# Optimization experiments

Measured on AMD Instinct MI355X. Metric: run time of the kernel, lower is better.

## Reference

```python
import jax, jax.numpy as jnp
import numpy as np

DMN_FACTOR = 0.5  # (2.0 - default_mode_network_activity=1.0) * 0.5, constant at default state


def setup_inputs() -> dict:
    key = jax.random.key(0)
    k1, k2, k3, k4 = jax.random.split(key, 4)
    B, H = 16384, 2048
    return {
        "x": jax.random.normal(k1, (B, H), dtype=jnp.float32),
        "W": jax.random.normal(k2, (H, H), dtype=jnp.float32) * (1.0 / np.sqrt(H)),
        "b": jnp.zeros((H,), dtype=jnp.float32),
        "plasticity_modulation": jax.random.uniform(k3, (H,), dtype=jnp.float32),
        "connectivity_mask": jax.random.uniform(k4, (H, H), dtype=jnp.float32),
    }


def reference(x, W, b, plasticity_modulation, connectivity_mask):
    H = x.shape[1]
    # trkb_signaling: Linear + Sigmoid
    bdnf_effect = jax.nn.sigmoid(x @ W.T + b)  # [B, H]
    # elementwise plasticity scaling
    xs = x * plasticity_modulation  # [B, H]
    # functional integration: mean_j(xs_i * xs_j * mask_ij) == xs * (mask @ xs^T)/H
    # (fused form of bmm outer-product * mask, mean over dim=2)
    fi = xs * (xs @ connectivity_mask.T) * (DMN_FACTOR / H)  # [B, H]
    return xs + bdnf_effect * fi
```

## Files before the change

kernel.cpp:

```cpp
#include <hip/hip_runtime.h>


#define M_DIM 16384
#define H_DIM 2048
#define BM 128
#define BN 128
#define BKB 128
#define NKT (H_DIM / BKB)
#define NTHREADS 512

typedef __attribute__((ext_vector_type(4))) int   intx4;
typedef __attribute__((ext_vector_type(8))) int   intx8;
typedef __attribute__((ext_vector_type(4))) float floatx4;

#define GPTR(p) ((const __attribute__((address_space(1))) void*)(p))
#define LPTR(p) ((__attribute__((address_space(3))) void*)(p))

__device__ __forceinline__ int pk4(float a, float b, float c, float d) {
    int v = __builtin_amdgcn_cvt_pk_fp8_f32(a, b, 0, false);
    v     = __builtin_amdgcn_cvt_pk_fp8_f32(c, d, v, true);
    return v;
}

__global__ void cvt_x8_kernel(const float* __restrict__ x,
                              unsigned char* __restrict__ x8, long n) {
    long stride = (long)gridDim.x * blockDim.x * 8;
    for (long j = ((long)blockIdx.x * blockDim.x + threadIdx.x) * 8; j < n; j += stride) {
        float4 v0 = *reinterpret_cast<const float4*>(x + j);
        float4 v1 = *reinterpret_cast<const float4*>(x + j + 4);
        int2 o;
        o.x = pk4(v0.x, v0.y, v0.z, v0.w);
        o.y = pk4(v1.x, v1.y, v1.z, v1.w);
        *reinterpret_cast<int2*>(x8 + j) = o;
    }
}

__global__ void cvt_wm8_kernel(const float* __restrict__ W,
                               const float* __restrict__ Mk,
                               const float* __restrict__ pm,
                               unsigned char* __restrict__ W8,
                               unsigned char* __restrict__ M8, long n) {
    long stride = (long)gridDim.x * blockDim.x * 8;
    for (long j = ((long)blockIdx.x * blockDim.x + threadIdx.x) * 8; j < n; j += stride) {
        float4 w0 = *reinterpret_cast<const float4*>(W + j);
        float4 w1 = *reinterpret_cast<const float4*>(W + j + 4);
        float4 m0 = *reinterpret_cast<const float4*>(Mk + j);
        float4 m1 = *reinterpret_cast<const float4*>(Mk + j + 4);
        const long col = j & (H_DIM - 1);
        float4 p0 = *reinterpret_cast<const float4*>(pm + col);
        float4 p1 = *reinterpret_cast<const float4*>(pm + col + 4);
        int2 ow, om;
        ow.x = pk4(w0.x * 16.f, w0.y * 16.f, w0.z * 16.f, w0.w * 16.f);
        ow.y = pk4(w1.x * 16.f, w1.y * 16.f, w1.z * 16.f, w1.w * 16.f);
        om.x = pk4(m0.x * p0.x * 16.f, m0.y * p0.y * 16.f,
                   m0.z * p0.z * 16.f, m0.w * p0.w * 16.f);
        om.y = pk4(m1.x * p1.x * 16.f, m1.y * p1.y * 16.f,
                   m1.z * p1.z * 16.f, m1.w * p1.w * 16.f);
        *reinterpret_cast<int2*>(W8 + j) = ow;
        *reinterpret_cast<int2*>(M8 + j) = om;
    }
}

__device__ __forceinline__ intx8 frag8(const unsigned char* s, int row, int g) {
    const unsigned char* p = s + row * BKB;
    const int c0 = ((2 * g)     ^ (row & 7)) * 16;
    const int c1 = ((2 * g + 1) ^ (row & 7)) * 16;
    intx4 lo = *reinterpret_cast<const intx4*>(p + c0);
    intx4 hi = *reinterpret_cast<const intx4*>(p + c1);
    return (intx8){lo.x, lo.y, lo.z, lo.w, hi.x, hi.y, hi.z, hi.w};
}

#define GLDS(src, dst) __builtin_amdgcn_global_load_lds(GPTR(src), LPTR(dst), 16, 0, 0)

#define STAGE_A(b, kt) do { \
    GLDS(gA0 + (kt),                       &sA[b][(srow     ) * BKB + scol_l]); \
    GLDS(gA0 + (kt) + (size_t)64  * H_DIM, &sA[b][(srow + 64) * BKB + scol_l]); } while (0)

#define STAGE_W(b, kt) do { \
    GLDS(gW0 + (kt),                       &sW[b][(srow     ) * BKB + scol_l]); \
    GLDS(gW0 + (kt) + (size_t)64  * H_DIM, &sW[b][(srow + 64) * BKB + scol_l]); } while (0)

#define STAGE_M(b, kt) do { \
    GLDS(gM0 + (kt),                       &sM[b][(srow     ) * BKB + scol_l]); \
    GLDS(gM0 + (kt) + (size_t)64  * H_DIM, &sM[b][(srow + 64) * BKB + scol_l]); } while (0)

#define BAR()  __builtin_amdgcn_s_barrier()
#define SBAR() __builtin_amdgcn_sched_barrier(0)
#define LGK0() do { asm volatile("s_waitcnt lgkmcnt(0)" ::: "memory"); SBAR(); } while (0)
#define VMC(n) asm volatile("s_waitcnt vmcnt(" #n ")" ::: "memory")
#define SGB(mask, n) __builtin_amdgcn_sched_group_barrier(mask, n, 0)

#define MFMASC(a, b, c) \
    __builtin_amdgcn_mfma_scale_f32_16x16x128_f8f6f4(a, b, c, 0, 0, 0, 127, 0, 123)

#define RD_A(dst, buf) do { \
    _Pragma("unroll") for (int m_ = 0; m_ < 4; ++m_) \
        dst[m_] = frag8(sA[buf], arow + m_ * 16, lg); } while (0)
#define RD_B(dst, sb, buf) do { \
    _Pragma("unroll") for (int n_ = 0; n_ < 2; ++n_) \
        dst[n_] = frag8(sb[buf], brw + n_ * 16, lg); } while (0)

#define MM(acc, av, bv) do { \
    _Pragma("unroll") for (int m_ = 0; m_ < 4; ++m_) \
    _Pragma("unroll") for (int n_ = 0; n_ < 2; ++n_) \
        acc[m_][n_] = MFMASC(av[m_], bv[n_], acc[m_][n_]); } while (0)

#define TILE(ct, nt, kst) do { \
    STAGE_A(nt, kst); STAGE_W(nt, kst); STAGE_M(nt, kst); \
    SBAR(); \
    RD_A(aF, ct); RD_B(bW, sW, ct); \
    LGK0(); \
    __builtin_amdgcn_s_setprio(1); \
    RD_B(bM, sM, ct); \
    MM(acc1, aF, bW); \
    _Pragma("unroll") for (int i_ = 0; i_ < 4; ++i_) { SGB(0x8, 1); SGB(0x100, 1); } \
    SGB(0x8, 4); \
    __builtin_amdgcn_s_setprio(0); \
    LGK0(); \
    __builtin_amdgcn_s_setprio(1); \
    MM(acc2, aF, bM); \
    __builtin_amdgcn_s_setprio(0); \
    SBAR(); \
    VMC(6); \
    BAR(); } while (0)

#define KOF(tt) (((tt) * BKB) & (H_DIM - 1))

__global__ __launch_bounds__(NTHREADS, 2)
void fused_gemm_kernel(const unsigned char* __restrict__ x8,
                       const unsigned char* __restrict__ W8,
                       const unsigned char* __restrict__ M8,
                       const float* __restrict__ x,
                       const float* __restrict__ bias,
                       const float* __restrict__ pm,
                       float* __restrict__ out) {
    __shared__ __align__(16) unsigned char sA[3][BM * BKB];
    __shared__ __align__(16) unsigned char sW[3][BN * BKB];
    __shared__ __align__(16) unsigned char sM[3][BN * BKB];

    const int t    = threadIdx.x;
    const int brow = blockIdx.y * BM;
    const int bcol = blockIdx.x * BN;

    const int srow   = t >> 3;
    const int chunk  = t & 7;
    const int scol_l = chunk * 16;
    const int scol_g = (chunk ^ (srow & 7)) * 16;

    const int w    = t >> 6;
    const int lane = t & 63;
    const int wr   = w >> 2;
    const int wc   = w & 3;
    const int lrow = lane & 15;
    const int lg   = lane >> 4;
    const int arow = wr * 64 + lrow;
    const int brw  = wc * 32 + lrow;

    floatx4 acc1[4][2], acc2[4][2];
#pragma unroll
    for (int m = 0; m < 4; ++m)
#pragma unroll
        for (int n = 0; n < 2; ++n) {
            acc1[m][n] = (floatx4){0.f, 0.f, 0.f, 0.f};
            acc2[m][n] = (floatx4){0.f, 0.f, 0.f, 0.f};
        }

    const unsigned char* gA0 = x8 + (size_t)(brow + srow) * H_DIM + scol_g;
    const unsigned char* gW0 = W8 + (size_t)(bcol + srow) * H_DIM + scol_g;
    const unsigned char* gM0 = M8 + (size_t)(bcol + srow) * H_DIM + scol_g;

    intx8 aF[4], bW[2], bM[2];

    STAGE_A(0, KOF(0)); STAGE_W(0, KOF(0)); STAGE_M(0, KOF(0));
    STAGE_A(1, KOF(1)); STAGE_W(1, KOF(1)); STAGE_M(1, KOF(1));
    VMC(6);
    BAR();

#pragma unroll 1
    for (int j = 0; j < 5; ++j) {
        const int t0 = 3 * j;
        TILE(0, 2, KOF(t0 + 2));
        TILE(1, 0, KOF(t0 + 3));
        TILE(2, 1, KOF(t0 + 4));
    }
    TILE(0, 2, KOF(17));

    const float c = 0.5f / (float)H_DIM;
#pragma unroll
    for (int n = 0; n < 2; ++n) {
        const int gcol = bcol + wc * 32 + n * 16 + lrow;
        const float bj  = bias[gcol];
        const float pmj = pm[gcol];
#pragma unroll
        for (int m = 0; m < 4; ++m) {
            floatx4 a1 = acc1[m][n];
            floatx4 a2 = acc2[m][n];
            const int growb = brow + wr * 64 + m * 16 + lg * 4;
#pragma unroll
            for (int r = 0; r < 4; ++r) {
                const size_t idx = (size_t)(growb + r) * H_DIM + gcol;
                const float xs  = x[idx] * pmj;
                const float s1  = a1[r] + bj;
                const float sig = 1.0f / (1.0f + __expf(-s1));
                out[idx] = xs + sig * (xs * a2[r] * c);
            }
        }
    }
}

extern "C" void kernel_launch(void* const* d_in, const int* in_sizes, int n_in,
                              void* d_out, int out_size, void* d_ws, size_t ws_size,
                              hipStream_t stream) {
    const float* x   = (const float*)d_in[0];
    const float* W   = (const float*)d_in[1];
    const float* b   = (const float*)d_in[2];
    const float* pm  = (const float*)d_in[3];
    const float* Mk  = (const float*)d_in[4];
    float* out = (float*)d_out;

    const long n_x = (long)M_DIM * H_DIM;
    const long n_w = (long)H_DIM * H_DIM;

    unsigned char* x8 = (unsigned char*)d_ws;
    unsigned char* W8 = x8 + n_x;
    unsigned char* M8 = W8 + n_w;

    cvt_x8_kernel<<<2048, 256, 0, stream>>>(x, x8, n_x);
    cvt_wm8_kernel<<<1024, 256, 0, stream>>>(W, Mk, pm, W8, M8, n_w);

    dim3 grid(H_DIM / BN, M_DIM / BM);
    fused_gemm_kernel<<<grid, NTHREADS, 0, stream>>>(x8, W8, M8, x, b, pm, out);
}
```

Measured before the change: 220.6 us.

## Pre-swizzle W and mask into MFMA fragment layout, load B directly to registers

```diff
diff --git a/kernel.cpp b/kernel.cpp
--- a/kernel.cpp
+++ b/kernel.cpp
@@ -8,6 +8,7 @@
 #define BKB 128
 #define NKT (H_DIM / BKB)
 #define NTHREADS 512
+#define FRAG_STRIDE 2048
 
 typedef __attribute__((ext_vector_type(4))) int   intx4;
 typedef __attribute__((ext_vector_type(8))) int   intx8;
@@ -35,30 +36,38 @@
     }
 }
 
-__global__ void cvt_wm8_kernel(const float* __restrict__ W,
-                               const float* __restrict__ Mk,
-                               const float* __restrict__ pm,
-                               unsigned char* __restrict__ W8,
-                               unsigned char* __restrict__ M8, long n) {
-    long stride = (long)gridDim.x * blockDim.x * 8;
-    for (long j = ((long)blockIdx.x * blockDim.x + threadIdx.x) * 8; j < n; j += stride) {
-        float4 w0 = *reinterpret_cast<const float4*>(W + j);
-        float4 w1 = *reinterpret_cast<const float4*>(W + j + 4);
-        float4 m0 = *reinterpret_cast<const float4*>(Mk + j);
-        float4 m1 = *reinterpret_cast<const float4*>(Mk + j + 4);
-        const long col = j & (H_DIM - 1);
-        float4 p0 = *reinterpret_cast<const float4*>(pm + col);
-        float4 p1 = *reinterpret_cast<const float4*>(pm + col + 4);
-        int2 ow, om;
-        ow.x = pk4(w0.x * 16.f, w0.y * 16.f, w0.z * 16.f, w0.w * 16.f);
-        ow.y = pk4(w1.x * 16.f, w1.y * 16.f, w1.z * 16.f, w1.w * 16.f);
-        om.x = pk4(m0.x * p0.x * 16.f, m0.y * p0.y * 16.f,
-                   m0.z * p0.z * 16.f, m0.w * p0.w * 16.f);
-        om.y = pk4(m1.x * p1.x * 16.f, m1.y * p1.y * 16.f,
-                   m1.z * p1.z * 16.f, m1.w * p1.w * 16.f);
-        *reinterpret_cast<int2*>(W8 + j) = ow;
-        *reinterpret_cast<int2*>(M8 + j) = om;
-    }
+__global__ void cvt_wm8f_kernel(const float* __restrict__ W,
+                                const float* __restrict__ Mk,
+                                const float* __restrict__ pm,
+                                unsigned char* __restrict__ W8f,
+                                unsigned char* __restrict__ M8f) {
+    const int tid = blockIdx.x * blockDim.x + threadIdx.x;
+    const int l   = tid & 63;
+    const int kt  = (tid >> 6) & (NKT - 1);
+    const int ct  = tid >> 10;
+    const int col = ct * 16 + (l & 15);
+    const int k0  = kt * 128 + (l >> 4) * 32;
+    const float* wsrc = W  + (size_t)col * H_DIM + k0;
+    const float* msrc = Mk + (size_t)col * H_DIM + k0;
+    const float* psrc = pm + k0;
+    int ow[8], om[8];
+#pragma unroll
+    for (int q = 0; q < 8; ++q) {
+        float4 wv = *reinterpret_cast<const float4*>(wsrc + q * 4);
+        float4 mv = *reinterpret_cast<const float4*>(msrc + q * 4);
+        float4 pv = *reinterpret_cast<const float4*>(psrc + q * 4);
+        ow[q] = pk4(wv.x * 16.f, wv.y * 16.f, wv.z * 16.f, wv.w * 16.f);
+        om[q] = pk4(mv.x * pv.x * 16.f, mv.y * pv.y * 16.f,
+                    mv.z * pv.z * 16.f, mv.w * pv.w * 16.f);
+    }
+    intx4 w0 = (intx4){ow[0], ow[1], ow[2], ow[3]};
+    intx4 w1 = (intx4){ow[4], ow[5], ow[6], ow[7]};
+    intx4 m0 = (intx4){om[0], om[1], om[2], om[3]};
+    intx4 m1 = (intx4){om[4], om[5], om[6], om[7]};
+    *reinterpret_cast<intx4*>(W8f + (size_t)tid * 32)      = w0;
+    *reinterpret_cast<intx4*>(W8f + (size_t)tid * 32 + 16) = w1;
+    *reinterpret_cast<intx4*>(M8f + (size_t)tid * 32)      = m0;
+    *reinterpret_cast<intx4*>(M8f + (size_t)tid * 32 + 16) = m1;
 }
 
 __device__ __forceinline__ intx8 frag8(const unsigned char* s, int row, int g) {
@@ -70,25 +79,22 @@
     return (intx8){lo.x, lo.y, lo.z, lo.w, hi.x, hi.y, hi.z, hi.w};
 }
 
+__device__ __forceinline__ intx8 ldb(const unsigned char* p) {
+    intx4 lo = *reinterpret_cast<const intx4*>(p);
+    intx4 hi = *reinterpret_cast<const intx4*>(p + 16);
+    return (intx8){lo.x, lo.y, lo.z, lo.w, hi.x, hi.y, hi.z, hi.w};
+}
+
 #define GLDS(src, dst) __builtin_amdgcn_global_load_lds(GPTR(src), LPTR(dst), 16, 0, 0)
 
 #define STAGE_A(b, kt) do { \
     GLDS(gA0 + (kt),                       &sA[b][(srow     ) * BKB + scol_l]); \
     GLDS(gA0 + (kt) + (size_t)64  * H_DIM, &sA[b][(srow + 64) * BKB + scol_l]); } while (0)
-
-#define STAGE_W(b, kt) do { \
-    GLDS(gW0 + (kt),                       &sW[b][(srow     ) * BKB + scol_l]); \
-    GLDS(gW0 + (kt) + (size_t)64  * H_DIM, &sW[b][(srow + 64) * BKB + scol_l]); } while (0)
-
-#define STAGE_M(b, kt) do { \
-    GLDS(gM0 + (kt),                       &sM[b][(srow     ) * BKB + scol_l]); \
-    GLDS(gM0 + (kt) + (size_t)64  * H_DIM, &sM[b][(srow + 64) * BKB + scol_l]); } while (0)
 
 #define BAR()  __builtin_amdgcn_s_barrier()
 #define SBAR() __builtin_amdgcn_sched_barrier(0)
 #define LGK0() do { asm volatile("s_waitcnt lgkmcnt(0)" ::: "memory"); SBAR(); } while (0)
 #define VMC(n) asm volatile("s_waitcnt vmcnt(" #n ")" ::: "memory")
-#define SGB(mask, n) __builtin_amdgcn_sched_group_barrier(mask, n, 0)
 
 #define MFMASC(a, b, c) \
     __builtin_amdgcn_mfma_scale_f32_16x16x128_f8f6f4(a, b, c, 0, 0, 0, 127, 0, 123)
@@ -96,47 +102,42 @@
 #define RD_A(dst, buf) do { \
     _Pragma("unroll") for (int m_ = 0; m_ < 4; ++m_) \
         dst[m_] = frag8(sA[buf], arow + m_ * 16, lg); } while (0)
-#define RD_B(dst, sb, buf) do { \
-    _Pragma("unroll") for (int n_ = 0; n_ < 2; ++n_) \
-        dst[n_] = frag8(sb[buf], brw + n_ * 16, lg); } while (0)
 
 #define MM(acc, av, bv) do { \
     _Pragma("unroll") for (int m_ = 0; m_ < 4; ++m_) \
     _Pragma("unroll") for (int n_ = 0; n_ < 2; ++n_) \
         acc[m_][n_] = MFMASC(av[m_], bv[n_], acc[m_][n_]); } while (0)
 
-#define TILE(ct, nt, kst) do { \
-    STAGE_A(nt, kst); STAGE_W(nt, kst); STAGE_M(nt, kst); \
-    SBAR(); \
-    RD_A(aF, ct); RD_B(bW, sW, ct); \
+#define KOF(tt) (((tt) * BKB) & (H_DIM - 1))
+
+#define TILE(ct_, nt_, tcur, tnext) do { \
+    bW[0] = ldb(bWb + (size_t)(tcur) * FRAG_STRIDE); \
+    bW[1] = ldb(bWb + (size_t)NKT * FRAG_STRIDE + (size_t)(tcur) * FRAG_STRIDE); \
+    SBAR(); \
+    bM[0] = ldb(bMb + (size_t)(tcur) * FRAG_STRIDE); \
+    bM[1] = ldb(bMb + (size_t)NKT * FRAG_STRIDE + (size_t)(tcur) * FRAG_STRIDE); \
+    SBAR(); \
+    STAGE_A(nt_, KOF(tnext)); \
+    SBAR(); \
+    RD_A(aF, ct_); \
     LGK0(); \
-    __builtin_amdgcn_s_setprio(1); \
-    RD_B(bM, sM, ct); \
-    MM(acc1, aF, bW); \
-    _Pragma("unroll") for (int i_ = 0; i_ < 4; ++i_) { SGB(0x8, 1); SGB(0x100, 1); } \
-    SGB(0x8, 4); \
-    __builtin_amdgcn_s_setprio(0); \
-    LGK0(); \
-    __builtin_amdgcn_s_setprio(1); \
-    MM(acc2, aF, bM); \
-    __builtin_amdgcn_s_setprio(0); \
-    SBAR(); \
     VMC(6); \
+    __builtin_amdgcn_s_setprio(1); MM(acc1, aF, bW); __builtin_amdgcn_s_setprio(0); \
+    VMC(2); \
+    __builtin_amdgcn_s_setprio(1); MM(acc2, aF, bM); __builtin_amdgcn_s_setprio(0); \
+    SBAR(); \
+    VMC(0); \
     BAR(); } while (0)
-
-#define KOF(tt) (((tt) * BKB) & (H_DIM - 1))
 
 __global__ __launch_bounds__(NTHREADS, 2)
 void fused_gemm_kernel(const unsigned char* __restrict__ x8,
-                       const unsigned char* __restrict__ W8,
-                       const unsigned char* __restrict__ M8,
+                       const unsigned char* __restrict__ W8f,
+                       const unsigned char* __restrict__ M8f,
                        const float* __restrict__ x,
                        const float* __restrict__ bias,
                        const float* __restrict__ pm,
                        float* __restrict__ out) {
-    __shared__ __align__(16) unsigned char sA[3][BM * BKB];
-    __shared__ __align__(16) unsigned char sW[3][BN * BKB];
-    __shared__ __align__(16) unsigned char sM[3][BN * BKB];
+    __shared__ __align__(16) unsigned char sA[2][BM * BKB];
 
     const int t    = threadIdx.x;
     const int brow = blockIdx.y * BM;
@@ -154,7 +155,6 @@
     const int lrow = lane & 15;
     const int lg   = lane >> 4;
     const int arow = wr * 64 + lrow;
-    const int brw  = wc * 32 + lrow;
 
     floatx4 acc1[4][2], acc2[4][2];
 #pragma unroll
@@ -166,24 +166,20 @@
         }
 
     const unsigned char* gA0 = x8 + (size_t)(brow + srow) * H_DIM + scol_g;
-    const unsigned char* gW0 = W8 + (size_t)(bcol + srow) * H_DIM + scol_g;
-    const unsigned char* gM0 = M8 + (size_t)(bcol + srow) * H_DIM + scol_g;
+    const unsigned char* bWb = W8f + ((size_t)(bcol / 16 + wc * 2) * NKT * 64 + lane) * 32;
+    const unsigned char* bMb = M8f + ((size_t)(bcol / 16 + wc * 2) * NKT * 64 + lane) * 32;
 
     intx8 aF[4], bW[2], bM[2];
 
-    STAGE_A(0, KOF(0)); STAGE_W(0, KOF(0)); STAGE_M(0, KOF(0));
-    STAGE_A(1, KOF(1)); STAGE_W(1, KOF(1)); STAGE_M(1, KOF(1));
-    VMC(6);
+    STAGE_A(0, KOF(0));
+    VMC(0);
     BAR();
 
 #pragma unroll 1
-    for (int j = 0; j < 5; ++j) {
-        const int t0 = 3 * j;
-        TILE(0, 2, KOF(t0 + 2));
-        TILE(1, 0, KOF(t0 + 3));
-        TILE(2, 1, KOF(t0 + 4));
-    }
-    TILE(0, 2, KOF(17));
+    for (int j = 0; j < NKT / 2; ++j) {
+        TILE(0, 1, 2 * j,     2 * j + 1);
+        TILE(1, 0, 2 * j + 1, 2 * j + 2);
+    }
 
     const float c = 0.5f / (float)H_DIM;
 #pragma unroll
@@ -221,13 +217,13 @@
     const long n_x = (long)M_DIM * H_DIM;
     const long n_w = (long)H_DIM * H_DIM;
 
-    unsigned char* x8 = (unsigned char*)d_ws;
-    unsigned char* W8 = x8 + n_x;
-    unsigned char* M8 = W8 + n_w;
+    unsigned char* x8  = (unsigned char*)d_ws;
+    unsigned char* W8f = x8 + n_x;
+    unsigned char* M8f = W8f + n_w;
 
     cvt_x8_kernel<<<2048, 256, 0, stream>>>(x, x8, n_x);
-    cvt_wm8_kernel<<<1024, 256, 0, stream>>>(W, Mk, pm, W8, M8, n_w);
+    cvt_wm8f_kernel<<<512, 256, 0, stream>>>(W, Mk, pm, W8f, M8f);
 
     dim3 grid(H_DIM / BN, M_DIM / BM);
-    fused_gemm_kernel<<<grid, NTHREADS, 0, stream>>>(x8, W8, M8, x, b, pm, out);
-}
+    fused_gemm_kernel<<<grid, NTHREADS, 0, stream>>>(x8, W8f, M8f, x, b, pm, out);
+}
```

Measured after the change: 233.2 us. 5.7% more time.
